# Optimization experiments

Measured on AMD Instinct MI355X. Metric: run time of the kernel, lower is better.

## Reference

```python
import jax, jax.numpy as jnp
import numpy as np

N_IN = 4096      # input features
N_NPB = 64       # neurons (inputs) per branch column
N_B = 64         # branches
N_NEXT_H = 256   # next hidden width
COLS = N_B * N_NEXT_H
BATCH = 128


def setup_inputs() -> dict:
    key = jax.random.key(0)
    k1, k2, k3 = jax.random.split(key, 3)
    x = jax.random.normal(k1, (BATCH, N_IN), dtype=jnp.float32)
    # torch kaiming_normal_ on (n_npb, cols): fan_in = cols, gain = sqrt(2)
    std = np.sqrt(2.0 / COLS).astype(np.float32)
    w = jax.random.normal(k2, (N_NPB, COLS), dtype=jnp.float32) * std
    # random per-column input indices (the module's all_branch_indices)
    idx = jax.random.randint(k3, (N_NPB, COLS), 0, N_IN, dtype=jnp.int32)
    return {"x": x, "w": w, "idx": idx}


def _last_write_mask(idx):
    # (row, col) targets. keep[k, c] is True iff no k' > k has idx[k', c] == idx[k, c].
    eq = idx[:, None, :] == idx[None, :, :]                    # [K, K, C]
    later = jnp.triu(jnp.ones((N_NPB, N_NPB), bool), 1)        # k' > k
    return ~jnp.any(eq & later[:, :, None], axis=1)            # [K, C]


def reference(x, w, idx):
    keep = _last_write_mask(idx)
    w_eff = jnp.where(keep, w, jnp.zeros((), x.dtype))         # [K, C]
    cols = jnp.broadcast_to(jnp.arange(COLS), (N_NPB, COLS))
    # scatter weights into dense [n_in, cols] (equals torch's clone+index_put)
    dense = jnp.zeros((N_IN, COLS), x.dtype).at[idx, cols].add(w_eff)
    out = x @ dense                                            # [B, COLS]
    return out.reshape(-1, N_B, N_NEXT_H)
```

## Files before the change

### kernel.cpp

```cpp
#include <hip/hip_runtime.h>

#define N_IN   4096
#define N_NPB  64
#define COLS   16384
#define BATCH  128

typedef unsigned int       uint;
typedef unsigned short     ushort;
typedef unsigned long long ulong64;


static __device__ __forceinline__ ushort f2bf(float f) {
  uint u = __float_as_uint(f);
  u += 0x7fffu + ((u >> 16) & 1u);
  return (ushort)(u >> 16);
}

__global__ __launch_bounds__(256) void transpose_bf16_kernel(
    const float* __restrict__ x, ushort* __restrict__ xTb) {
  __shared__ float tile[32][33];
  const int i0 = blockIdx.x * 32;
  const int b0 = blockIdx.y * 32;
  const int tx = threadIdx.x;
  const int ty = threadIdx.y;
#pragma unroll
  for (int j = 0; j < 32; j += 8)
    tile[ty + j][tx] = x[(b0 + ty + j) * N_IN + i0 + tx];
  __syncthreads();
#pragma unroll
  for (int j = 0; j < 32; j += 8)
    xTb[(i0 + ty + j) * BATCH + b0 + tx] = f2bf(tile[tx][ty + j]);
}

template <int KBASE>
static __device__ __forceinline__ uint compute_bits(const int* __restrict__ ip) {
  int v[64 - KBASE];
#pragma unroll
  for (int k = 0; k < 64 - KBASE; ++k) v[k] = ip[(KBASE + k) * COLS];
  uint bits = 0;
#pragma unroll
  for (int j = 0; j < 16; ++j) {
    uint m = 0xffffffffu;
#pragma unroll
    for (int kp = j + 1; kp < 64 - KBASE; ++kp)
      m = min(m, (uint)(v[j] ^ v[kp]));
    bits |= (m != 0u) ? (1u << j) : 0u;
  }
  return bits;
}

__global__ __launch_bounds__(256, 4) void keepmask_kernel(
    const int* __restrict__ idx, ushort* __restrict__ keep16) {
  const int tid = threadIdx.x;
  const int kg  = __builtin_amdgcn_readfirstlane(tid >> 6);
  const int c   = blockIdx.x * 64 + (tid & 63);
  const int* ip = idx + c;
  uint bits;
  if      (kg == 0) bits = compute_bits<0>(ip);
  else if (kg == 1) bits = compute_bits<16>(ip);
  else if (kg == 2) bits = compute_bits<32>(ip);
  else              bits = compute_bits<48>(ip);
  keep16[c * 4 + kg] = (ushort)bits;
}

__global__ __launch_bounds__(256, 4) void branch_main_kernel(
    const float* __restrict__ w, const int* __restrict__ idx,
    const ulong64* __restrict__ keep, const ushort* __restrict__ xTb,
    float* __restrict__ out) {
  __shared__ float wlds[N_NPB][17];
  __shared__ float res[BATCH][17];

  const int tid = threadIdx.x;
  const int c0  = blockIdx.x * 16;

  {
    const int cl = tid & 15;
    const ulong64 km = keep[c0 + cl];
    const int k0 = tid >> 4;
#pragma unroll
    for (int p = 0; p < 4; ++p) {
      const int k = k0 + p * 16;
      const float wv = w[k * COLS + c0 + cl];
      wlds[k][cl] = ((km >> k) & 1ull) ? wv : 0.0f;
    }
  }
  __syncthreads();

  const int wave = tid >> 6;
  const int lane = tid & 63;
  const int g    = lane >> 4;
  const int b8   = lane & 15;
  const int cl   = wave * 4 + g;
  const int c    = c0 + cl;

  int rows[64];
  {
    const int* ip = idx + c;
#pragma unroll
    for (int k = 0; k < 64; ++k) rows[k] = ip[k * COLS];
  }

  float a0 = 0.f, a1 = 0.f, a2 = 0.f, a3 = 0.f;
  float a4 = 0.f, a5 = 0.f, a6 = 0.f, a7 = 0.f;
  const char* xb = (const char*)xTb;
  const uint  bo = (uint)b8 * 16;

#pragma unroll
  for (int k = 0; k < 64; ++k) {
    const uint4 u = *(const uint4*)(xb + (((uint)rows[k] << 8) + bo));
    const float wv = wlds[k][cl];
    a0 = fmaf(wv, __uint_as_float(u.x << 16),          a0);
    a1 = fmaf(wv, __uint_as_float(u.x & 0xffff0000u),  a1);
    a2 = fmaf(wv, __uint_as_float(u.y << 16),          a2);
    a3 = fmaf(wv, __uint_as_float(u.y & 0xffff0000u),  a3);
    a4 = fmaf(wv, __uint_as_float(u.z << 16),          a4);
    a5 = fmaf(wv, __uint_as_float(u.z & 0xffff0000u),  a5);
    a6 = fmaf(wv, __uint_as_float(u.w << 16),          a6);
    a7 = fmaf(wv, __uint_as_float(u.w & 0xffff0000u),  a7);
  }

  res[b8 * 8 + 0][cl] = a0;
  res[b8 * 8 + 1][cl] = a1;
  res[b8 * 8 + 2][cl] = a2;
  res[b8 * 8 + 3][cl] = a3;
  res[b8 * 8 + 4][cl] = a4;
  res[b8 * 8 + 5][cl] = a5;
  res[b8 * 8 + 6][cl] = a6;
  res[b8 * 8 + 7][cl] = a7;
  __syncthreads();

  for (int e = tid; e < BATCH * 16; e += 256) {
    out[(e >> 4) * COLS + c0 + (e & 15)] = res[e >> 4][e & 15];
  }
}

extern "C" void kernel_launch(void* const* d_in, const int* in_sizes, int n_in,
                              void* d_out, int out_size, void* d_ws, size_t ws_size,
                              hipStream_t stream) {
  const float* x   = (const float*)d_in[0];
  const float* w   = (const float*)d_in[1];
  const int*   idx = (const int*)d_in[2];
  float* out = (float*)d_out;

  char* ws = (char*)d_ws;
  ushort*  xTb    = (ushort*)(ws);
  ushort*  keep16 = (ushort*)(ws + (1u << 20));
  ulong64* keep   = (ulong64*)(ws + (1u << 20));

  hipLaunchKernelGGL(transpose_bf16_kernel, dim3(N_IN / 32, BATCH / 32),
                     dim3(32, 8), 0, stream, x, xTb);
  hipLaunchKernelGGL(keepmask_kernel, dim3(COLS / 64), dim3(256), 0, stream,
                     idx, keep16);
  hipLaunchKernelGGL(branch_main_kernel, dim3(COLS / 16), dim3(256), 0, stream,
                     w, idx, keep, xTb, out);
}
```

Before: 29.68 us.

## Fuse prep kernels and switch main gather-FMA to packed fp16 math

Merges the transpose and keep-mask kernels into one launch, with block ranges picking the role. Converts x to fp16 instead of bf16 and does the inner product with packed half2 multiply-adds, accumulating in fp16. Weights and row offsets are packed together into shared memory, so each thread no longer holds 64 row indices in registers, and the occupancy hint is raised to 8. Accumulating 64 terms in fp16 risks precision loss relative to the fp32 reference.

```diff
diff --git a/kernel.cpp b/kernel.cpp
--- a/kernel.cpp
+++ b/kernel.cpp
@@ -7,30 +7,9 @@
 
 typedef unsigned int       uint;
 typedef unsigned short     ushort;
-typedef unsigned long long ulong64;
+typedef unsigned long long u64;
+typedef __attribute__((ext_vector_type(2))) _Float16 h2;
 
-
-static __device__ __forceinline__ ushort f2bf(float f) {
-  uint u = __float_as_uint(f);
-  u += 0x7fffu + ((u >> 16) & 1u);
-  return (ushort)(u >> 16);
-}
-
-__global__ __launch_bounds__(256) void transpose_bf16_kernel(
-    const float* __restrict__ x, ushort* __restrict__ xTb) {
-  __shared__ float tile[32][33];
-  const int i0 = blockIdx.x * 32;
-  const int b0 = blockIdx.y * 32;
-  const int tx = threadIdx.x;
-  const int ty = threadIdx.y;
-#pragma unroll
-  for (int j = 0; j < 32; j += 8)
-    tile[ty + j][tx] = x[(b0 + ty + j) * N_IN + i0 + tx];
-  __syncthreads();
-#pragma unroll
-  for (int j = 0; j < 32; j += 8)
-    xTb[(i0 + ty + j) * BATCH + b0 + tx] = f2bf(tile[tx][ty + j]);
-}
 
 template <int KBASE>
 static __device__ __forceinline__ uint compute_bits(const int* __restrict__ ip) {
@@ -49,39 +28,60 @@
   return bits;
 }
 
-__global__ __launch_bounds__(256, 4) void keepmask_kernel(
-    const int* __restrict__ idx, ushort* __restrict__ keep16) {
+__global__ __launch_bounds__(256, 4) void prep_kernel(
+    const float* __restrict__ x, const int* __restrict__ idx,
+    ushort* __restrict__ xTh, ushort* __restrict__ keep16) {
+  const int bid = blockIdx.x;
   const int tid = threadIdx.x;
-  const int kg  = __builtin_amdgcn_readfirstlane(tid >> 6);
-  const int c   = blockIdx.x * 64 + (tid & 63);
-  const int* ip = idx + c;
-  uint bits;
-  if      (kg == 0) bits = compute_bits<0>(ip);
-  else if (kg == 1) bits = compute_bits<16>(ip);
-  else if (kg == 2) bits = compute_bits<32>(ip);
-  else              bits = compute_bits<48>(ip);
-  keep16[c * 4 + kg] = (ushort)bits;
+  if (bid < 512) {
+    __shared__ float tile[32][33];
+    const int i0 = (bid & 127) * 32;
+    const int b0 = (bid >> 7) * 32;
+    const int tx = tid & 31;
+    const int ty = tid >> 5;
+#pragma unroll
+    for (int j = 0; j < 32; j += 8)
+      tile[ty + j][tx] = x[(b0 + ty + j) * N_IN + i0 + tx];
+    __syncthreads();
+#pragma unroll
+    for (int j = 0; j < 32; j += 8)
+      xTh[(i0 + ty + j) * BATCH + b0 + tx] =
+          __builtin_bit_cast(ushort, (_Float16)tile[tx][ty + j]);
+  } else {
+    const int kg = __builtin_amdgcn_readfirstlane(tid >> 6);
+    const int c  = (bid - 512) * 64 + (tid & 63);
+    const int* ip = idx + c;
+    uint bits;
+    if      (kg == 0) bits = compute_bits<0>(ip);
+    else if (kg == 1) bits = compute_bits<16>(ip);
+    else if (kg == 2) bits = compute_bits<32>(ip);
+    else              bits = compute_bits<48>(ip);
+    keep16[c * 4 + kg] = (ushort)bits;
+  }
 }
 
-__global__ __launch_bounds__(256, 4) void branch_main_kernel(
+__global__ __launch_bounds__(256, 8) void branch_main_kernel(
     const float* __restrict__ w, const int* __restrict__ idx,
-    const ulong64* __restrict__ keep, const ushort* __restrict__ xTb,
+    const u64* __restrict__ keep, const ushort* __restrict__ xTh,
     float* __restrict__ out) {
-  __shared__ float wlds[N_NPB][17];
-  __shared__ float res[BATCH][17];
+  __shared__ u64   pk[N_NPB][16];
+  __shared__ float res2[16][129];
 
   const int tid = threadIdx.x;
   const int c0  = blockIdx.x * 16;
 
   {
     const int cl = tid & 15;
-    const ulong64 km = keep[c0 + cl];
-    const int k0 = tid >> 4;
+    const int k0 = (tid >> 4) * 4;
+    const u64 km = keep[c0 + cl];
 #pragma unroll
     for (int p = 0; p < 4; ++p) {
-      const int k = k0 + p * 16;
-      const float wv = w[k * COLS + c0 + cl];
-      wlds[k][cl] = ((km >> k) & 1ull) ? wv : 0.0f;
+      const int k   = k0 + p;
+      const int row = idx[k * COLS + c0 + cl];
+      float wv      = w[k * COLS + c0 + cl];
+      wv = ((km >> k) & 1ull) ? wv : 0.0f;
+      const uint hb = (uint)__builtin_bit_cast(ushort, (_Float16)wv);
+      pk[k][cl] = ((u64)((hb << 16) | hb) << 32) | ((u64)((uint)row << 8));
     }
   }
   __syncthreads();
@@ -91,46 +91,35 @@
   const int g    = lane >> 4;
   const int b8   = lane & 15;
   const int cl   = wave * 4 + g;
-  const int c    = c0 + cl;
 
-  int rows[64];
-  {
-    const int* ip = idx + c;
-#pragma unroll
-    for (int k = 0; k < 64; ++k) rows[k] = ip[k * COLS];
-  }
-
-  float a0 = 0.f, a1 = 0.f, a2 = 0.f, a3 = 0.f;
-  float a4 = 0.f, a5 = 0.f, a6 = 0.f, a7 = 0.f;
-  const char* xb = (const char*)xTb;
+  h2 a0 = (h2)0.0f, a1 = (h2)0.0f, a2 = (h2)0.0f, a3 = (h2)0.0f;
+  const char* xb = (const char*)xTh;
   const uint  bo = (uint)b8 * 16;
 
 #pragma unroll
-  for (int k = 0; k < 64; ++k) {
-    const uint4 u = *(const uint4*)(xb + (((uint)rows[k] << 8) + bo));
-    const float wv = wlds[k][cl];
-    a0 = fmaf(wv, __uint_as_float(u.x << 16),          a0);
-    a1 = fmaf(wv, __uint_as_float(u.x & 0xffff0000u),  a1);
-    a2 = fmaf(wv, __uint_as_float(u.y << 16),          a2);
-    a3 = fmaf(wv, __uint_as_float(u.y & 0xffff0000u),  a3);
-    a4 = fmaf(wv, __uint_as_float(u.z << 16),          a4);
-    a5 = fmaf(wv, __uint_as_float(u.z & 0xffff0000u),  a5);
-    a6 = fmaf(wv, __uint_as_float(u.w << 16),          a6);
-    a7 = fmaf(wv, __uint_as_float(u.w & 0xffff0000u),  a7);
+  for (int k = 0; k < N_NPB; ++k) {
+    const u64  e   = pk[k][cl];
+    const uint off = (uint)e;
+    const h2   wh  = __builtin_bit_cast(h2, (uint)(e >> 32));
+    const uint4 u  = *(const uint4*)(xb + off + bo);
+    a0 += __builtin_bit_cast(h2, u.x) * wh;
+    a1 += __builtin_bit_cast(h2, u.y) * wh;
+    a2 += __builtin_bit_cast(h2, u.z) * wh;
+    a3 += __builtin_bit_cast(h2, u.w) * wh;
   }
 
-  res[b8 * 8 + 0][cl] = a0;
-  res[b8 * 8 + 1][cl] = a1;
-  res[b8 * 8 + 2][cl] = a2;
-  res[b8 * 8 + 3][cl] = a3;
-  res[b8 * 8 + 4][cl] = a4;
-  res[b8 * 8 + 5][cl] = a5;
-  res[b8 * 8 + 6][cl] = a6;
-  res[b8 * 8 + 7][cl] = a7;
+  {
+    float* r = &res2[cl][b8 * 8];
+    r[0] = (float)a0.x; r[1] = (float)a0.y;
+    r[2] = (float)a1.x; r[3] = (float)a1.y;
+    r[4] = (float)a2.x; r[5] = (float)a2.y;
+    r[6] = (float)a3.x; r[7] = (float)a3.y;
+  }
   __syncthreads();
 
   for (int e = tid; e < BATCH * 16; e += 256) {
-    out[(e >> 4) * COLS + c0 + (e & 15)] = res[e >> 4][e & 15];
+    const int b = e >> 4, cc = e & 15;
+    out[b * COLS + c0 + cc] = res2[cc][b];
   }
 }
 
@@ -143,14 +132,12 @@
   float* out = (float*)d_out;
 
   char* ws = (char*)d_ws;
-  ushort*  xTb    = (ushort*)(ws);
-  ushort*  keep16 = (ushort*)(ws + (1u << 20));
-  ulong64* keep   = (ulong64*)(ws + (1u << 20));
+  ushort* xTh    = (ushort*)(ws);
+  ushort* keep16 = (ushort*)(ws + (1u << 20));
+  u64*    keep   = (u64*)(ws + (1u << 20));
 
-  hipLaunchKernelGGL(transpose_bf16_kernel, dim3(N_IN / 32, BATCH / 32),
-                     dim3(32, 8), 0, stream, x, xTb);
-  hipLaunchKernelGGL(keepmask_kernel, dim3(COLS / 64), dim3(256), 0, stream,
-                     idx, keep16);
+  hipLaunchKernelGGL(prep_kernel, dim3(512 + COLS / 64), dim3(256), 0, stream,
+                     x, idx, xTh, keep16);
   hipLaunchKernelGGL(branch_main_kernel, dim3(COLS / 16), dim3(256), 0, stream,
-                     w, idx, keep, xTb, out);
+                     w, idx, keep, xTh, out);
 }
```

New measurement: 23.91 us. 19.5% less time.
